# Performance work log

Hardware: AMD Instinct MI355X
Metric: run time of the kernel (lower is better)

The kernel has to match this reference:

```python
import jax, jax.numpy as jnp
import numpy as np

BS, N_OPS, N_JOBS, N_MA, E, H = 256, 2000, 50, 40, 128, 128


def setup_inputs() -> dict:
    key = jax.random.key(0)
    ks = jax.random.split(key, 12)
    return {
        "ops_emb": jax.random.normal(ks[0], (BS, N_OPS, E), jnp.float32),
        "ma_emb": jax.random.normal(ks[1], (BS, N_MA, E), jnp.float32),
        "next_op": jax.random.randint(ks[2], (BS, N_JOBS), 0, N_OPS),
        "action_mask": jnp.ones((BS, N_JOBS * N_MA + 1), dtype=bool),
        "dummy": jax.random.normal(ks[3], (2 * E,), jnp.float32),
        "W1": jax.random.normal(ks[4], (2 * E, H), jnp.float32) * 0.05,
        "b1": jax.random.normal(ks[5], (H,), jnp.float32) * 0.05,
        "W2": jax.random.normal(ks[6], (H, H), jnp.float32) * 0.05,
        "b2": jax.random.normal(ks[7], (H,), jnp.float32) * 0.05,
        "W3": jax.random.normal(ks[8], (H, 1), jnp.float32) * 0.05,
        "b3": jax.random.normal(ks[9], (1,), jnp.float32) * 0.05,
    }


def reference(ops_emb, ma_emb, next_op, action_mask, dummy, W1, b1, W2, b2, W3, b3):
    bs, n_ma = ma_emb.shape[:2]
    e = ma_emb.shape[-1]
    # gather_by_index: job_emb [bs, n_jobs, E]
    job_emb = jnp.take_along_axis(ops_emb, next_op[..., None], axis=1)
    # Fused broadcast-concat + first linear: cat(job, ma) @ W1 == job @ W1[:E] + ma @ W1[E:]
    Wj, Wm = W1[:e], W1[e:]
    job_proj = jnp.einsum("bje,eh->bjh", job_emb, Wj)  # [bs, n_jobs, H]
    ma_proj = jnp.einsum("bme,eh->bmh", ma_emb, Wm)    # [bs, n_ma, H]
    h1 = jax.nn.relu(job_proj[:, :, None, :] + ma_proj[:, None, :, :] + b1)  # [bs, nj, nm, H]
    h2 = jax.nn.relu(jnp.einsum("bjmh,hk->bjmk", h1, W2) + b2)
    pair_logits = (jnp.einsum("bjmh,ho->bjmo", h2, W3) + b3)[..., 0]  # [bs, nj, nm]
    pair_logits = pair_logits.reshape(bs, -1)
    # no-op logit from dummy vector through the same MLP
    d1 = jax.nn.relu(dummy @ W1 + b1)
    d2 = jax.nn.relu(d1 @ W2 + b2)
    noop = (d2 @ W3 + b3)  # [1]
    noop = jnp.broadcast_to(noop[None, :], (bs, 1))
    logits = jnp.concatenate([noop, pair_logits], axis=1)  # [bs, nj*nm+1]
    return logits, action_mask
```

## Files before the change

### kernel.cpp

```cpp
#include <hip/hip_runtime.h>
#include <hip/hip_bf16.h>

#define BS_   256
#define NOPS_ 2000
#define NJ_   50
#define NM_   40
#define E_    128
#define H_    128
#define NCOL_ 2001

typedef _Float16 f16;
using f16x8 = __attribute__((ext_vector_type(8))) _Float16;
using f32x4 = __attribute__((ext_vector_type(4))) float;

__global__ __launch_bounds__(512, 2) void fjsp_fused(
    const float* __restrict__ ops_emb,
    const float* __restrict__ ma_emb,
    const int*   __restrict__ next_op,
    const int*   __restrict__ amask,
    const float* __restrict__ dummy,
    const float* __restrict__ W1,
    const float* __restrict__ b1,
    const float* __restrict__ W2,
    const float* __restrict__ b2,
    const float* __restrict__ W3,
    const float* __restrict__ b3,
    float* __restrict__ out)
{
  const int b    = blockIdx.x;
  const int tid  = threadIdx.x;
  const int lane = tid & 63;
  const int wave = tid >> 6;
  const int g    = lane >> 4;
  const int lr   = lane & 15;

  __shared__ __align__(16) f16 jpL[NJ_][136];
  __shared__ __align__(16) f16 mpL[NM_][136];
  __shared__ float d1s[128];
  __shared__ float noopL;

  if (wave < 7) {
    const int phase = (wave < 4) ? 0 : 1;
    const int r0 = (phase ? (wave - 4) : wave) * 16;

    f16x8 af[4];
    {
      const float4* ep;
      if (phase == 0) {
        int jr = r0 + lr; if (jr > NJ_ - 1) jr = NJ_ - 1;
        const int idx = next_op[b * NJ_ + jr];
        ep = reinterpret_cast<const float4*>(ops_emb + ((size_t)b * NOPS_ + idx) * E_);
      } else {
        int mr = r0 + lr; if (mr > NM_ - 1) mr = NM_ - 1;
        ep = reinterpret_cast<const float4*>(ma_emb + ((size_t)b * NM_ + mr) * E_);
      }
      #pragma unroll
      for (int f = 0; f < 4; ++f) {
        const float4 v0 = ep[8 * f + 2 * g];
        const float4 v1 = ep[8 * f + 2 * g + 1];
        f16x8 a;
        a[0] = (f16)v0.x; a[1] = (f16)v0.y; a[2] = (f16)v0.z; a[3] = (f16)v0.w;
        a[4] = (f16)v1.x; a[5] = (f16)v1.y; a[6] = (f16)v1.z; a[7] = (f16)v1.w;
        af[f] = a;
      }
    }

    f32x4 acc[8];
    #pragma unroll
    for (int c = 0; c < 8; ++c) {
      const float binit = phase ? b1[16 * c + lr] : 0.f;
      acc[c] = f32x4{binit, binit, binit, binit};
    }
    const int ebase = phase ? E_ : 0;
    #pragma unroll
    for (int f = 0; f < 4; ++f) {
      #pragma unroll
      for (int c = 0; c < 8; ++c) {
        const float* wp = W1 + (size_t)(ebase + 32 * f + 8 * g) * H_ + 16 * c + lr;
        f16x8 bb;
        #pragma unroll
        for (int i = 0; i < 8; ++i) bb[i] = (f16)wp[(size_t)i * H_];
        acc[c] = __builtin_amdgcn_mfma_f32_16x16x32_f16(af[f], bb, acc[c], 0, 0, 0);
      }
    }
    #pragma unroll
    for (int c = 0; c < 8; ++c) {
      const int col = 16 * c + lr;
      #pragma unroll
      for (int i = 0; i < 4; ++i) {
        const int row = r0 + 4 * g + i;
        if (phase == 0) { if (row < NJ_) jpL[row][col] = (f16)acc[c][i]; }
        else            { if (row < NM_) mpL[row][col] = (f16)acc[c][i]; }
      }
    }
  } else {
    float s0 = 0.f, s1 = 0.f;
    #pragma unroll 8
    for (int e = 0; e < 2 * E_; ++e) {
      const float dv = dummy[e];
      s0 = fmaf(dv, W1[(size_t)e * H_ + lane],      s0);
      s1 = fmaf(dv, W1[(size_t)e * H_ + 64 + lane], s1);
    }
    d1s[lane]      = fmaxf(s0 + b1[lane],      0.f);
    d1s[64 + lane] = fmaxf(s1 + b1[64 + lane], 0.f);
    asm volatile("s_waitcnt lgkmcnt(0)" ::: "memory");
    __builtin_amdgcn_wave_barrier();
    float t0 = 0.f, t1 = 0.f;
    #pragma unroll 8
    for (int k = 0; k < H_; ++k) {
      const float dk = d1s[k];
      t0 = fmaf(dk, W2[(size_t)k * H_ + lane],      t0);
      t1 = fmaf(dk, W2[(size_t)k * H_ + 64 + lane], t1);
    }
    float nv = fmaxf(t0 + b2[lane],      0.f) * W3[lane]
             + fmaxf(t1 + b2[64 + lane], 0.f) * W3[64 + lane];
    #pragma unroll
    for (int s = 1; s < 64; s <<= 1) nv += __shfl_xor(nv, s);
    if (lane == 0) noopL = nv + b3[0];
  }

  f16x8 w2f[4][8];
  #pragma unroll
  for (int f = 0; f < 4; ++f) {
    #pragma unroll
    for (int c = 0; c < 8; ++c) {
      const float* wp = W2 + (size_t)(32 * f + 8 * g) * H_ + 16 * c + lr;
      f16x8 bb;
      #pragma unroll
      for (int i = 0; i < 8; ++i) bb[i] = (f16)wp[(size_t)i * H_];
      w2f[f][c] = bb;
    }
  }
  float b2r[8], w3r[8];
  #pragma unroll
  for (int c = 0; c < 8; ++c) { b2r[c] = b2[16 * c + lr]; w3r[c] = W3[16 * c + lr]; }
  const float bias3 = b3[0];

  __syncthreads();

  float* __restrict__ outrow = out + (size_t)b * NCOL_ + 1;

  #pragma unroll 1
  for (int t = wave; t < 125; t += 8) {
    const int tp0  = t * 16;
    const int rowr = tp0 + lr;
    const int j = rowr / 40;
    const int m = rowr - j * 40;
    f16x8 afr[4];
    #pragma unroll
    for (int f = 0; f < 4; ++f) {
      const f16x8 jv = *reinterpret_cast<const f16x8*>(&jpL[j][32 * f + 8 * g]);
      const f16x8 mv = *reinterpret_cast<const f16x8*>(&mpL[m][32 * f + 8 * g]);
      const f16x8 s  = jv + mv;
      afr[f] = __builtin_elementwise_max(s, (f16x8)(f16)0.0f);
    }
    f32x4 acc[8];
    #pragma unroll
    for (int c = 0; c < 8; ++c)
      acc[c] = f32x4{b2r[c], b2r[c], b2r[c], b2r[c]};
    #pragma unroll
    for (int f = 0; f < 4; ++f)
      #pragma unroll
      for (int c = 0; c < 8; ++c)
        acc[c] = __builtin_amdgcn_mfma_f32_16x16x32_f16(afr[f], w2f[f][c], acc[c], 0, 0, 0);
    float p0v = 0.f, p1v = 0.f, p2v = 0.f, p3v = 0.f;
    #pragma unroll
    for (int c = 0; c < 8; ++c) {
      p0v = fmaf(fmaxf(acc[c][0], 0.f), w3r[c], p0v);
      p1v = fmaf(fmaxf(acc[c][1], 0.f), w3r[c], p1v);
      p2v = fmaf(fmaxf(acc[c][2], 0.f), w3r[c], p2v);
      p3v = fmaf(fmaxf(acc[c][3], 0.f), w3r[c], p3v);
    }
    #pragma unroll
    for (int s = 1; s < 16; s <<= 1) {
      p0v += __shfl_xor(p0v, s);
      p1v += __shfl_xor(p1v, s);
      p2v += __shfl_xor(p2v, s);
      p3v += __shfl_xor(p3v, s);
    }
    if (lr == 0) {
      const int row = tp0 + 4 * g;
      outrow[row + 0] = p0v + bias3;
      outrow[row + 1] = p1v + bias3;
      outrow[row + 2] = p2v + bias3;
      outrow[row + 3] = p3v + bias3;
    }
  }

  {
    const int* mrow = amask + (size_t)b * NCOL_;
    float* __restrict__ orow = out + (size_t)BS_ * NCOL_ + (size_t)b * NCOL_;
    for (int i = tid; i < NCOL_; i += 512) orow[i] = mrow[i] != 0 ? 1.0f : 0.0f;
  }

  if (tid == 0) out[(size_t)b * NCOL_] = noopL;
}

extern "C" void kernel_launch(void* const* d_in, const int* in_sizes, int n_in,
                              void* d_out, int out_size, void* d_ws, size_t ws_size,
                              hipStream_t stream) {
  (void)in_sizes; (void)n_in; (void)d_ws; (void)ws_size; (void)out_size;
  fjsp_fused<<<dim3(BS_), dim3(512), 0, stream>>>(
      (const float*)d_in[0],
      (const float*)d_in[1],
      (const int*)d_in[2],
      (const int*)d_in[3],
      (const float*)d_in[4],
      (const float*)d_in[5],
      (const float*)d_in[6],
      (const float*)d_in[7],
      (const float*)d_in[8],
      (const float*)d_in[9],
      (const float*)d_in[10],
      (float*)d_out);
}
```

Baseline: 38.25 us.

## Split each batch row across two 256-thread blocks and transpose the second MFMA

Launches two blocks of 256 threads per batch element instead of one block of 512, each handling half of the job-machine tiles and half of the mask copy. Both blocks recompute the job and machine projections and the no-op MLP, so first-layer work is duplicated in exchange for more, smaller blocks across the CUs. The second-layer MFMA swaps its operands so each lane holds outputs for a single pair, which shortens the W3 reduction to two shuffles and lets one store per pair replace four. The no-op MLP loops also gain multiple accumulators to shorten dependency chains.

```diff
diff --git a/kernel.cpp b/kernel.cpp
--- a/kernel.cpp
+++ b/kernel.cpp
@@ -13,7 +13,7 @@
 using f16x8 = __attribute__((ext_vector_type(8))) _Float16;
 using f32x4 = __attribute__((ext_vector_type(4))) float;
 
-__global__ __launch_bounds__(512, 2) void fjsp_fused(
+__global__ __launch_bounds__(256, 2) void fjsp_fused(
     const float* __restrict__ ops_emb,
     const float* __restrict__ ma_emb,
     const int*   __restrict__ next_op,
@@ -27,7 +27,9 @@
     const float* __restrict__ b3,
     float* __restrict__ out)
 {
-  const int b    = blockIdx.x;
+  const int bid  = blockIdx.x;
+  const int b    = bid >> 1;
+  const int sub  = bid & 1;
   const int tid  = threadIdx.x;
   const int lane = tid & 63;
   const int wave = tid >> 6;
@@ -37,46 +39,31 @@
   __shared__ __align__(16) f16 jpL[NJ_][136];
   __shared__ __align__(16) f16 mpL[NM_][136];
   __shared__ float d1s[128];
-  __shared__ float noopL;
-
-  if (wave < 7) {
-    const int phase = (wave < 4) ? 0 : 1;
-    const int r0 = (phase ? (wave - 4) : wave) * 16;
-
+
+  {
+    const int r0 = wave * 16;
+    int jr = r0 + lr; if (jr > NJ_ - 1) jr = NJ_ - 1;
+    const int idx = next_op[b * NJ_ + jr];
+    const float4* ep = reinterpret_cast<const float4*>(
+        ops_emb + ((size_t)b * NOPS_ + idx) * E_);
     f16x8 af[4];
-    {
-      const float4* ep;
-      if (phase == 0) {
-        int jr = r0 + lr; if (jr > NJ_ - 1) jr = NJ_ - 1;
-        const int idx = next_op[b * NJ_ + jr];
-        ep = reinterpret_cast<const float4*>(ops_emb + ((size_t)b * NOPS_ + idx) * E_);
-      } else {
-        int mr = r0 + lr; if (mr > NM_ - 1) mr = NM_ - 1;
-        ep = reinterpret_cast<const float4*>(ma_emb + ((size_t)b * NM_ + mr) * E_);
-      }
-      #pragma unroll
-      for (int f = 0; f < 4; ++f) {
-        const float4 v0 = ep[8 * f + 2 * g];
-        const float4 v1 = ep[8 * f + 2 * g + 1];
-        f16x8 a;
-        a[0] = (f16)v0.x; a[1] = (f16)v0.y; a[2] = (f16)v0.z; a[3] = (f16)v0.w;
-        a[4] = (f16)v1.x; a[5] = (f16)v1.y; a[6] = (f16)v1.z; a[7] = (f16)v1.w;
-        af[f] = a;
-      }
-    }
-
+    #pragma unroll
+    for (int f = 0; f < 4; ++f) {
+      const float4 v0 = ep[8 * f + 2 * g];
+      const float4 v1 = ep[8 * f + 2 * g + 1];
+      f16x8 a;
+      a[0] = (f16)v0.x; a[1] = (f16)v0.y; a[2] = (f16)v0.z; a[3] = (f16)v0.w;
+      a[4] = (f16)v1.x; a[5] = (f16)v1.y; a[6] = (f16)v1.z; a[7] = (f16)v1.w;
+      af[f] = a;
+    }
     f32x4 acc[8];
     #pragma unroll
-    for (int c = 0; c < 8; ++c) {
-      const float binit = phase ? b1[16 * c + lr] : 0.f;
-      acc[c] = f32x4{binit, binit, binit, binit};
-    }
-    const int ebase = phase ? E_ : 0;
+    for (int c = 0; c < 8; ++c) acc[c] = f32x4{0.f, 0.f, 0.f, 0.f};
     #pragma unroll
     for (int f = 0; f < 4; ++f) {
       #pragma unroll
       for (int c = 0; c < 8; ++c) {
-        const float* wp = W1 + (size_t)(ebase + 32 * f + 8 * g) * H_ + 16 * c + lr;
+        const float* wp = W1 + (size_t)(32 * f + 8 * g) * H_ + 16 * c + lr;
         f16x8 bb;
         #pragma unroll
         for (int i = 0; i < 8; ++i) bb[i] = (f16)wp[(size_t)i * H_];
@@ -89,34 +76,82 @@
       #pragma unroll
       for (int i = 0; i < 4; ++i) {
         const int row = r0 + 4 * g + i;
-        if (phase == 0) { if (row < NJ_) jpL[row][col] = (f16)acc[c][i]; }
-        else            { if (row < NM_) mpL[row][col] = (f16)acc[c][i]; }
+        if (row < NJ_) jpL[row][col] = (f16)acc[c][i];
+      }
+    }
+  }
+
+  if (wave < 3) {
+    const int r0 = wave * 16;
+    int mr = r0 + lr; if (mr > NM_ - 1) mr = NM_ - 1;
+    const float4* ep = reinterpret_cast<const float4*>(
+        ma_emb + ((size_t)b * NM_ + mr) * E_);
+    f16x8 af[4];
+    #pragma unroll
+    for (int f = 0; f < 4; ++f) {
+      const float4 v0 = ep[8 * f + 2 * g];
+      const float4 v1 = ep[8 * f + 2 * g + 1];
+      f16x8 a;
+      a[0] = (f16)v0.x; a[1] = (f16)v0.y; a[2] = (f16)v0.z; a[3] = (f16)v0.w;
+      a[4] = (f16)v1.x; a[5] = (f16)v1.y; a[6] = (f16)v1.z; a[7] = (f16)v1.w;
+      af[f] = a;
+    }
+    f32x4 acc[8];
+    #pragma unroll
+    for (int c = 0; c < 8; ++c) {
+      const float binit = b1[16 * c + lr];
+      acc[c] = f32x4{binit, binit, binit, binit};
+    }
+    #pragma unroll
+    for (int f = 0; f < 4; ++f) {
+      #pragma unroll
+      for (int c = 0; c < 8; ++c) {
+        const float* wp = W1 + (size_t)(E_ + 32 * f + 8 * g) * H_ + 16 * c + lr;
+        f16x8 bb;
+        #pragma unroll
+        for (int i = 0; i < 8; ++i) bb[i] = (f16)wp[(size_t)i * H_];
+        acc[c] = __builtin_amdgcn_mfma_f32_16x16x32_f16(af[f], bb, acc[c], 0, 0, 0);
+      }
+    }
+    #pragma unroll
+    for (int c = 0; c < 8; ++c) {
+      const int col = 16 * c + lr;
+      #pragma unroll
+      for (int i = 0; i < 4; ++i) {
+        const int row = r0 + 4 * g + i;
+        if (row < NM_) mpL[row][col] = (f16)acc[c][i];
       }
     }
   } else {
-    float s0 = 0.f, s1 = 0.f;
-    #pragma unroll 8
-    for (int e = 0; e < 2 * E_; ++e) {
-      const float dv = dummy[e];
-      s0 = fmaf(dv, W1[(size_t)e * H_ + lane],      s0);
-      s1 = fmaf(dv, W1[(size_t)e * H_ + 64 + lane], s1);
-    }
-    d1s[lane]      = fmaxf(s0 + b1[lane],      0.f);
-    d1s[64 + lane] = fmaxf(s1 + b1[64 + lane], 0.f);
+    float s0[4] = {0,0,0,0}, s1[4] = {0,0,0,0};
+    #pragma unroll 2
+    for (int e = 0; e < 2 * E_; e += 4) {
+      #pragma unroll
+      for (int q = 0; q < 4; ++q) {
+        const float dv = dummy[e + q];
+        s0[q] = fmaf(dv, W1[(size_t)(e + q) * H_ + lane],      s0[q]);
+        s1[q] = fmaf(dv, W1[(size_t)(e + q) * H_ + 64 + lane], s1[q]);
+      }
+    }
+    d1s[lane]      = fmaxf(s0[0]+s0[1]+s0[2]+s0[3] + b1[lane],      0.f);
+    d1s[64 + lane] = fmaxf(s1[0]+s1[1]+s1[2]+s1[3] + b1[64 + lane], 0.f);
     asm volatile("s_waitcnt lgkmcnt(0)" ::: "memory");
     __builtin_amdgcn_wave_barrier();
-    float t0 = 0.f, t1 = 0.f;
-    #pragma unroll 8
-    for (int k = 0; k < H_; ++k) {
-      const float dk = d1s[k];
-      t0 = fmaf(dk, W2[(size_t)k * H_ + lane],      t0);
-      t1 = fmaf(dk, W2[(size_t)k * H_ + 64 + lane], t1);
-    }
-    float nv = fmaxf(t0 + b2[lane],      0.f) * W3[lane]
-             + fmaxf(t1 + b2[64 + lane], 0.f) * W3[64 + lane];
+    float t0[4] = {0,0,0,0}, t1[4] = {0,0,0,0};
+    #pragma unroll 2
+    for (int k = 0; k < H_; k += 4) {
+      #pragma unroll
+      for (int q = 0; q < 4; ++q) {
+        const float dk = d1s[k + q];
+        t0[q] = fmaf(dk, W2[(size_t)(k + q) * H_ + lane],      t0[q]);
+        t1[q] = fmaf(dk, W2[(size_t)(k + q) * H_ + 64 + lane], t1[q]);
+      }
+    }
+    float nv = fmaxf(t0[0]+t0[1]+t0[2]+t0[3] + b2[lane],      0.f) * W3[lane]
+             + fmaxf(t1[0]+t1[1]+t1[2]+t1[3] + b2[64 + lane], 0.f) * W3[64 + lane];
     #pragma unroll
     for (int s = 1; s < 64; s <<= 1) nv += __shfl_xor(nv, s);
-    if (lane == 0) noopL = nv + b3[0];
+    if (sub == 0 && lane == 0) out[(size_t)b * NCOL_] = nv + b3[0];
   }
 
   f16x8 w2f[4][8];
@@ -131,21 +166,26 @@
       w2f[f][c] = bb;
     }
   }
-  float b2r[8], w3r[8];
+  float4 b2v[8], w3v[8];
   #pragma unroll
-  for (int c = 0; c < 8; ++c) { b2r[c] = b2[16 * c + lr]; w3r[c] = W3[16 * c + lr]; }
+  for (int c = 0; c < 8; ++c) {
+    b2v[c] = *reinterpret_cast<const float4*>(b2 + 16 * c + 4 * g);
+    w3v[c] = *reinterpret_cast<const float4*>(W3 + 16 * c + 4 * g);
+  }
   const float bias3 = b3[0];
 
   __syncthreads();
 
   float* __restrict__ outrow = out + (size_t)b * NCOL_ + 1;
+  const int tstart = sub ? 63 : 0;
+  const int tend   = sub ? 125 : 63;
 
   #pragma unroll 1
-  for (int t = wave; t < 125; t += 8) {
+  for (int t = tstart + wave; t < tend; t += 4) {
     const int tp0  = t * 16;
-    const int rowr = tp0 + lr;
-    const int j = rowr / 40;
-    const int m = rowr - j * 40;
+    const int pair = tp0 + lr;
+    const int j = pair / 40;
+    const int m = pair - j * 40;
     f16x8 afr[4];
     #pragma unroll
     for (int f = 0; f < 4; ++f) {
@@ -157,50 +197,39 @@
     f32x4 acc[8];
     #pragma unroll
     for (int c = 0; c < 8; ++c)
-      acc[c] = f32x4{b2r[c], b2r[c], b2r[c], b2r[c]};
+      acc[c] = f32x4{b2v[c].x, b2v[c].y, b2v[c].z, b2v[c].w};
     #pragma unroll
     for (int f = 0; f < 4; ++f)
       #pragma unroll
       for (int c = 0; c < 8; ++c)
-        acc[c] = __builtin_amdgcn_mfma_f32_16x16x32_f16(afr[f], w2f[f][c], acc[c], 0, 0, 0);
-    float p0v = 0.f, p1v = 0.f, p2v = 0.f, p3v = 0.f;
-    #pragma unroll
-    for (int c = 0; c < 8; ++c) {
-      p0v = fmaf(fmaxf(acc[c][0], 0.f), w3r[c], p0v);
-      p1v = fmaf(fmaxf(acc[c][1], 0.f), w3r[c], p1v);
-      p2v = fmaf(fmaxf(acc[c][2], 0.f), w3r[c], p2v);
-      p3v = fmaf(fmaxf(acc[c][3], 0.f), w3r[c], p3v);
-    }
-    #pragma unroll
-    for (int s = 1; s < 16; s <<= 1) {
-      p0v += __shfl_xor(p0v, s);
-      p1v += __shfl_xor(p1v, s);
-      p2v += __shfl_xor(p2v, s);
-      p3v += __shfl_xor(p3v, s);
-    }
-    if (lr == 0) {
-      const int row = tp0 + 4 * g;
-      outrow[row + 0] = p0v + bias3;
-      outrow[row + 1] = p1v + bias3;
-      outrow[row + 2] = p2v + bias3;
-      outrow[row + 3] = p3v + bias3;
-    }
+        acc[c] = __builtin_amdgcn_mfma_f32_16x16x32_f16(w2f[f][c], afr[f], acc[c], 0, 0, 0);
+    float p = 0.f;
+    #pragma unroll
+    for (int c = 0; c < 8; ++c) {
+      p = fmaf(fmaxf(acc[c][0], 0.f), w3v[c].x, p);
+      p = fmaf(fmaxf(acc[c][1], 0.f), w3v[c].y, p);
+      p = fmaf(fmaxf(acc[c][2], 0.f), w3v[c].z, p);
+      p = fmaf(fmaxf(acc[c][3], 0.f), w3v[c].w, p);
+    }
+    p += __shfl_xor(p, 16);
+    p += __shfl_xor(p, 32);
+    if (g == 0) outrow[pair] = p + bias3;
   }
 
   {
     const int* mrow = amask + (size_t)b * NCOL_;
     float* __restrict__ orow = out + (size_t)BS_ * NCOL_ + (size_t)b * NCOL_;
-    for (int i = tid; i < NCOL_; i += 512) orow[i] = mrow[i] != 0 ? 1.0f : 0.0f;
-  }
-
-  if (tid == 0) out[(size_t)b * NCOL_] = noopL;
+    const int i0 = sub ? 1001 : 0;
+    const int i1 = sub ? NCOL_ : 1001;
+    for (int i = i0 + tid; i < i1; i += 256) orow[i] = mrow[i] != 0 ? 1.0f : 0.0f;
+  }
 }
 
 extern "C" void kernel_launch(void* const* d_in, const int* in_sizes, int n_in,
                               void* d_out, int out_size, void* d_ws, size_t ws_size,
                               hipStream_t stream) {
   (void)in_sizes; (void)n_in; (void)d_ws; (void)ws_size; (void)out_size;
-  fjsp_fused<<<dim3(BS_), dim3(512), 0, stream>>>(
+  fjsp_fused<<<dim3(BS_ * 2), dim3(256), 0, stream>>>(
       (const float*)d_in[0],
       (const float*)d_in[1],
       (const int*)d_in[2],
```

After: 43.49 us. 13.7% more time.

## Fold noop into pair tiles, share W2 fragments via LDS, transpose MFMA

Applied to the files above, without the earlier changes.

The dummy vector becomes an extra job row and an extra machine row, so the no-op logit is computed as pair 2000 inside the main MFMA loop instead of by a dedicated scalar wave. W2 is converted to f16 fragments once per block by two waves and staged in LDS, rather than every wave loading and converting it from global memory. The layer-2 MFMA operands are swapped so each lane's accumulator holds hidden units for a single pair, which cuts the W3 reduction to two shuffles. Mask conversion moves to a separate wave that overlaps the projection phase. The trade-off is one extra tile iteration, 32 KB of added LDS, and a projection phase spread unevenly across fewer waves.

```diff
diff --git a/kernel.cpp b/kernel.cpp
--- a/kernel.cpp
+++ b/kernel.cpp
@@ -11,6 +11,7 @@
 
 typedef _Float16 f16;
 using f16x8 = __attribute__((ext_vector_type(8))) _Float16;
+using f16x4 = __attribute__((ext_vector_type(4))) _Float16;
 using f32x4 = __attribute__((ext_vector_type(4))) float;
 
 __global__ __launch_bounds__(512, 2) void fjsp_fused(
@@ -34,26 +35,45 @@
   const int g    = lane >> 4;
   const int lr   = lane & 15;
 
-  __shared__ __align__(16) f16 jpL[NJ_][136];
-  __shared__ __align__(16) f16 mpL[NM_][136];
-  __shared__ float d1s[128];
-  __shared__ float noopL;
-
-  if (wave < 7) {
-    const int phase = (wave < 4) ? 0 : 1;
-    const int r0 = (phase ? (wave - 4) : wave) * 16;
-
-    f16x8 af[4];
-    {
-      const float4* ep;
-      if (phase == 0) {
-        int jr = r0 + lr; if (jr > NJ_ - 1) jr = NJ_ - 1;
-        const int idx = next_op[b * NJ_ + jr];
-        ep = reinterpret_cast<const float4*>(ops_emb + ((size_t)b * NOPS_ + idx) * E_);
+  __shared__ __align__(16) f16 fragL[32 * 64 * 8];
+  __shared__ __align__(16) f16 jpL[51][140];
+  __shared__ __align__(16) f16 mpL[41][140];
+
+  if (wave < 4) {
+    const bool  isJ   = (wave < 2);
+    const size_t ebase = isJ ? 0 : (size_t)E_ * H_;
+    f16x8 wfr[4][8];
+    #pragma unroll
+    for (int f = 0; f < 4; ++f) {
+      #pragma unroll
+      for (int c = 0; c < 8; ++c) {
+        const float* wp = W1 + ebase + (size_t)(32 * f + 8 * g) * H_ + 16 * c + lr;
+        f16x8 bb;
+        #pragma unroll
+        for (int i = 0; i < 8; ++i) bb[i] = (f16)wp[(size_t)i * H_];
+        wfr[f][c] = bb;
+      }
+    }
+    float b1r[8];
+    #pragma unroll
+    for (int c = 0; c < 8; ++c) b1r[c] = isJ ? 0.f : b1[16 * c + lr];
+
+    const int t0 = (wave == 0) ? 0 : (wave == 1) ? 2 : (wave == 2) ? 0 : 2;
+    const int nt = (wave == 3) ? 1 : 2;
+    for (int q = 0; q < nt; ++q) {
+      const int r0 = (t0 + q) * 16;
+      const float* src;
+      if (isJ) {
+        int jr = r0 + lr; if (jr > 50) jr = 50;
+        src = (jr == 50) ? dummy
+                         : ops_emb + ((size_t)b * NOPS_ + next_op[b * NJ_ + jr]) * E_;
       } else {
-        int mr = r0 + lr; if (mr > NM_ - 1) mr = NM_ - 1;
-        ep = reinterpret_cast<const float4*>(ma_emb + ((size_t)b * NM_ + mr) * E_);
-      }
+        int mr = r0 + lr; if (mr > 40) mr = 40;
+        src = (mr == 40) ? (dummy + E_)
+                         : ma_emb + ((size_t)b * NM_ + mr) * E_;
+      }
+      const float4* ep = reinterpret_cast<const float4*>(src);
+      f16x8 af[4];
       #pragma unroll
       for (int f = 0; f < 4; ++f) {
         const float4 v0 = ep[8 * f + 2 * g];
@@ -63,137 +83,101 @@
         a[4] = (f16)v1.x; a[5] = (f16)v1.y; a[6] = (f16)v1.z; a[7] = (f16)v1.w;
         af[f] = a;
       }
-    }
-
-    f32x4 acc[8];
-    #pragma unroll
-    for (int c = 0; c < 8; ++c) {
-      const float binit = phase ? b1[16 * c + lr] : 0.f;
-      acc[c] = f32x4{binit, binit, binit, binit};
-    }
-    const int ebase = phase ? E_ : 0;
-    #pragma unroll
-    for (int f = 0; f < 4; ++f) {
+      f32x4 acc[8];
+      #pragma unroll
+      for (int c = 0; c < 8; ++c) acc[c] = f32x4{b1r[c], b1r[c], b1r[c], b1r[c]};
+      #pragma unroll
+      for (int f = 0; f < 4; ++f)
+        #pragma unroll
+        for (int c = 0; c < 8; ++c)
+          acc[c] = __builtin_amdgcn_mfma_f32_16x16x32_f16(af[f], wfr[f][c], acc[c], 0, 0, 0);
       #pragma unroll
       for (int c = 0; c < 8; ++c) {
-        const float* wp = W1 + (size_t)(ebase + 32 * f + 8 * g) * H_ + 16 * c + lr;
-        f16x8 bb;
+        const int col = 16 * c + lr;
         #pragma unroll
-        for (int i = 0; i < 8; ++i) bb[i] = (f16)wp[(size_t)i * H_];
-        acc[c] = __builtin_amdgcn_mfma_f32_16x16x32_f16(af[f], bb, acc[c], 0, 0, 0);
-      }
-    }
-    #pragma unroll
-    for (int c = 0; c < 8; ++c) {
-      const int col = 16 * c + lr;
-      #pragma unroll
-      for (int i = 0; i < 4; ++i) {
-        const int row = r0 + 4 * g + i;
-        if (phase == 0) { if (row < NJ_) jpL[row][col] = (f16)acc[c][i]; }
-        else            { if (row < NM_) mpL[row][col] = (f16)acc[c][i]; }
-      }
-    }
-  } else {
-    float s0 = 0.f, s1 = 0.f;
-    #pragma unroll 8
-    for (int e = 0; e < 2 * E_; ++e) {
-      const float dv = dummy[e];
-      s0 = fmaf(dv, W1[(size_t)e * H_ + lane],      s0);
-      s1 = fmaf(dv, W1[(size_t)e * H_ + 64 + lane], s1);
-    }
-    d1s[lane]      = fmaxf(s0 + b1[lane],      0.f);
-    d1s[64 + lane] = fmaxf(s1 + b1[64 + lane], 0.f);
-    asm volatile("s_waitcnt lgkmcnt(0)" ::: "memory");
-    __builtin_amdgcn_wave_barrier();
-    float t0 = 0.f, t1 = 0.f;
-    #pragma unroll 8
-    for (int k = 0; k < H_; ++k) {
-      const float dk = d1s[k];
-      t0 = fmaf(dk, W2[(size_t)k * H_ + lane],      t0);
-      t1 = fmaf(dk, W2[(size_t)k * H_ + 64 + lane], t1);
-    }
-    float nv = fmaxf(t0 + b2[lane],      0.f) * W3[lane]
-             + fmaxf(t1 + b2[64 + lane], 0.f) * W3[64 + lane];
-    #pragma unroll
-    for (int s = 1; s < 64; s <<= 1) nv += __shfl_xor(nv, s);
-    if (lane == 0) noopL = nv + b3[0];
+        for (int i = 0; i < 4; ++i) {
+          const int row = r0 + 4 * g + i;
+          if (isJ) { if (row < 51) jpL[row][col] = (f16)acc[c][i]; }
+          else     { if (row < 41) mpL[row][col] = (f16)acc[c][i]; }
+        }
+      }
+    }
+  } else if (wave < 6) {
+    #pragma unroll 4
+    for (int q = 0; q < 16; ++q) {
+      const int t = (wave - 4) * 16 + q;
+      const int f = t >> 3, c = t & 7;
+      const float* wp = W2 + (size_t)(32 * f + 8 * g) * H_ + 16 * c + lr;
+      f16x8 bb;
+      #pragma unroll
+      for (int i = 0; i < 8; ++i) bb[i] = (f16)wp[(size_t)i * H_];
+      *reinterpret_cast<f16x8*>(&fragL[((size_t)t * 64 + lane) * 8]) = bb;
+    }
+  } else if (wave == 7) {
+    const int* mrow = amask + (size_t)b * NCOL_;
+    float* __restrict__ orow = out + (size_t)BS_ * NCOL_ + (size_t)b * NCOL_;
+    #pragma unroll 4
+    for (int i = lane; i < NCOL_; i += 64) orow[i] = mrow[i] != 0 ? 1.0f : 0.0f;
   }
+  __syncthreads();
 
   f16x8 w2f[4][8];
   #pragma unroll
-  for (int f = 0; f < 4; ++f) {
+  for (int f = 0; f < 4; ++f)
+    #pragma unroll
+    for (int c = 0; c < 8; ++c)
+      w2f[f][c] = *reinterpret_cast<const f16x8*>(
+          &fragL[((size_t)(f * 8 + c) * 64 + lane) * 8]);
+  float4 b2v[8], w3v[8];
+  #pragma unroll
+  for (int c = 0; c < 8; ++c) {
+    b2v[c] = *reinterpret_cast<const float4*>(b2 + 16 * c + 4 * g);
+    w3v[c] = *reinterpret_cast<const float4*>(W3 + 16 * c + 4 * g);
+  }
+  const float bias3 = b3[0];
+  float* __restrict__ outb = out + (size_t)b * NCOL_;
+
+  #pragma unroll 1
+  for (int t = wave; t < 126; t += 8) {
+    const int p  = t * 16 + lr;
+    const int p2 = (p < 2000) ? p : 2000;
+    int j, m;
+    if (p2 == 2000) { j = 50; m = 40; }
+    else            { j = p2 / 40; m = p2 - j * 40; }
+    f16x8 afr[4];
+    #pragma unroll
+    for (int f = 0; f < 4; ++f) {
+      const f16x4 jlo = *reinterpret_cast<const f16x4*>(&jpL[j][32 * f + 8 * g]);
+      const f16x4 jhi = *reinterpret_cast<const f16x4*>(&jpL[j][32 * f + 8 * g + 4]);
+      const f16x4 mlo = *reinterpret_cast<const f16x4*>(&mpL[m][32 * f + 8 * g]);
+      const f16x4 mhi = *reinterpret_cast<const f16x4*>(&mpL[m][32 * f + 8 * g + 4]);
+      const f16x4 z   = {(f16)0.f, (f16)0.f, (f16)0.f, (f16)0.f};
+      const f16x4 slo = __builtin_elementwise_max(jlo + mlo, z);
+      const f16x4 shi = __builtin_elementwise_max(jhi + mhi, z);
+      afr[f] = __builtin_shufflevector(slo, shi, 0, 1, 2, 3, 4, 5, 6, 7);
+    }
+    f32x4 acc[8];
+    #pragma unroll
+    for (int c = 0; c < 8; ++c)
+      acc[c] = f32x4{b2v[c].x, b2v[c].y, b2v[c].z, b2v[c].w};
+    #pragma unroll
+    for (int f = 0; f < 4; ++f)
+      #pragma unroll
+      for (int c = 0; c < 8; ++c)
+        acc[c] = __builtin_amdgcn_mfma_f32_16x16x32_f16(w2f[f][c], afr[f], acc[c], 0, 0, 0);
+    float pv = 0.f;
     #pragma unroll
     for (int c = 0; c < 8; ++c) {
-      const float* wp = W2 + (size_t)(32 * f + 8 * g) * H_ + 16 * c + lr;
-      f16x8 bb;
-      #pragma unroll
-      for (int i = 0; i < 8; ++i) bb[i] = (f16)wp[(size_t)i * H_];
-      w2f[f][c] = bb;
-    }
+      pv = fmaf(fmaxf(acc[c][0], 0.f), w3v[c].x, pv);
+      pv = fmaf(fmaxf(acc[c][1], 0.f), w3v[c].y, pv);
+      pv = fmaf(fmaxf(acc[c][2], 0.f), w3v[c].z, pv);
+      pv = fmaf(fmaxf(acc[c][3], 0.f), w3v[c].w, pv);
+    }
+    pv += __shfl_xor(pv, 16);
+    pv += __shfl_xor(pv, 32);
+    if (g == 0 && p <= 2000)
+      outb[(p == 2000) ? 0 : (p + 1)] = pv + bias3;
   }
-  float b2r[8], w3r[8];
-  #pragma unroll
-  for (int c = 0; c < 8; ++c) { b2r[c] = b2[16 * c + lr]; w3r[c] = W3[16 * c + lr]; }
-  const float bias3 = b3[0];
-
-  __syncthreads();
-
-  float* __restrict__ outrow = out + (size_t)b * NCOL_ + 1;
-
-  #pragma unroll 1
-  for (int t = wave; t < 125; t += 8) {
-    const int tp0  = t * 16;
-    const int rowr = tp0 + lr;
-    const int j = rowr / 40;
-    const int m = rowr - j * 40;
-    f16x8 afr[4];
-    #pragma unroll
-    for (int f = 0; f < 4; ++f) {
-      const f16x8 jv = *reinterpret_cast<const f16x8*>(&jpL[j][32 * f + 8 * g]);
-      const f16x8 mv = *reinterpret_cast<const f16x8*>(&mpL[m][32 * f + 8 * g]);
-      const f16x8 s  = jv + mv;
-      afr[f] = __builtin_elementwise_max(s, (f16x8)(f16)0.0f);
-    }
-    f32x4 acc[8];
-    #pragma unroll
-    for (int c = 0; c < 8; ++c)
-      acc[c] = f32x4{b2r[c], b2r[c], b2r[c], b2r[c]};
-    #pragma unroll
-    for (int f = 0; f < 4; ++f)
-      #pragma unroll
-      for (int c = 0; c < 8; ++c)
-        acc[c] = __builtin_amdgcn_mfma_f32_16x16x32_f16(afr[f], w2f[f][c], acc[c], 0, 0, 0);
-    float p0v = 0.f, p1v = 0.f, p2v = 0.f, p3v = 0.f;
-    #pragma unroll
-    for (int c = 0; c < 8; ++c) {
-      p0v = fmaf(fmaxf(acc[c][0], 0.f), w3r[c], p0v);
-      p1v = fmaf(fmaxf(acc[c][1], 0.f), w3r[c], p1v);
-      p2v = fmaf(fmaxf(acc[c][2], 0.f), w3r[c], p2v);
-      p3v = fmaf(fmaxf(acc[c][3], 0.f), w3r[c], p3v);
-    }
-    #pragma unroll
-    for (int s = 1; s < 16; s <<= 1) {
-      p0v += __shfl_xor(p0v, s);
-      p1v += __shfl_xor(p1v, s);
-      p2v += __shfl_xor(p2v, s);
-      p3v += __shfl_xor(p3v, s);
-    }
-    if (lr == 0) {
-      const int row = tp0 + 4 * g;
-      outrow[row + 0] = p0v + bias3;
-      outrow[row + 1] = p1v + bias3;
-      outrow[row + 2] = p2v + bias3;
-      outrow[row + 3] = p3v + bias3;
-    }
-  }
-
-  {
-    const int* mrow = amask + (size_t)b * NCOL_;
-    float* __restrict__ orow = out + (size_t)BS_ * NCOL_ + (size_t)b * NCOL_;
-    for (int i = tid; i < NCOL_; i += 512) orow[i] = mrow[i] != 0 ? 1.0f : 0.0f;
-  }
-
-  if (tid == 0) out[(size_t)b * NCOL_] = noopL;
 }
 
 extern "C" void kernel_launch(void* const* d_in, const int* in_sizes, int n_in,
```

New measurement: 36.72 us. 1.04x faster.
